# Performance work log

Measured on AMD Instinct MI355X. Metric: run time of the kernel, lower is better.

The kernel has to match this reference:

```python
import jax, jax.numpy as jnp
import numpy as np
import math

# dims: batch, seq_len, d_model, heads, head_dim
B, L, DM, H, DH = 1, 4096, 1024, 16, 64
BS, W, MAXD, DFF = 64, 16, 256, 4096  # block_size, band width (blocks), max rel distance, ffn dim
NB = L // BS


def _static_layout():
    # Static block-sparse causal band layout: tgt block n attends to src blocks [n-W+1 .. n].
    # Mirrors construct_blocksparse_rel_ids: rel = tgt_pos - src_pos, pos ids start at 1
    # (0 reserved for padding), clamp rel<-1 -> -1, rel>max_distance -> max_distance, then +1.
    n = np.arange(NB)[:, None, None, None]
    w = np.arange(W)[None, :, None, None]
    i = np.arange(BS)[None, None, :, None]
    j = np.arange(BS)[None, None, None, :]
    src_blk = n - (W - 1) + w
    # valid: block exists; diagonal block (w==W-1) is causal within-block (j<=i)
    valid = (src_blk >= 0) & ((w < W - 1) | (j <= i))
    tgt_pos = n * BS + i + 1
    src_pos = np.clip(src_blk, 0, None) * BS + j + 1
    rel = np.clip(tgt_pos - src_pos, -1, MAXD) + 1
    rel = np.where(valid, rel, 0)  # masked positions get rel id 0 (as in masked_fill_)
    src_idx = np.clip(np.arange(NB)[:, None] - (W - 1) + np.arange(W)[None, :], 0, None)
    return jnp.asarray(rel), jnp.asarray(valid), jnp.asarray(src_idx)

REL_IDS, VALID, SRC_IDX = _static_layout()  # [NB,W,BS,BS], [NB,W,BS,BS], [NB,W]


def _ln(x, g, b):
    m = x.mean(-1, keepdims=True)
    v = ((x - m) ** 2).mean(-1, keepdims=True)
    return (x - m) * jax.lax.rsqrt(v + 1e-5) * g + b


def setup_inputs() -> dict:
    key = jax.random.key(0)
    ks = jax.random.split(key, 10)
    p = lambda k, shape: jax.random.normal(k, shape, jnp.float32) * 0.02
    return dict(
        x=jax.random.normal(ks[0], (B, L, DM), jnp.float32),
        Wq=p(ks[1], (DM, DM)), Wk=p(ks[2], (DM, DM)), Wv=p(ks[3], (DM, DM)),
        Wo=p(ks[4], (DM, DM)),
        rel_emb=p(ks[5], (MAXD + 2, H)),  # per-head relative position bias table
        ln1_g=jnp.ones((DM,), jnp.float32), ln1_b=jnp.zeros((DM,), jnp.float32),
        ln2_g=jnp.ones((DM,), jnp.float32), ln2_b=jnp.zeros((DM,), jnp.float32),
        W1=p(ks[6], (DM, DFF)), b1=jnp.zeros((DFF,), jnp.float32),
        W2=p(ks[7], (DFF, DM)), b2=jnp.zeros((DM,), jnp.float32),
    )


def reference(x, Wq, Wk, Wv, Wo, rel_emb, ln1_g, ln1_b, ln2_g, ln2_b, W1, b1, W2, b2):
    h = _ln(x, ln1_g, ln1_b)

    def heads(Wt):
        return (h @ Wt).reshape(B, NB, BS, H, DH).transpose(0, 3, 1, 2, 4)  # [B,H,NB,BS,DH]

    q, k, v = heads(Wq), heads(Wk), heads(Wv)
    k_band = k[:, :, SRC_IDX]  # gather nonzero src blocks -> [B,H,NB,W,BS,DH]
    v_band = v[:, :, SRC_IDX]
    scores = jnp.einsum('bhnid,bhnwjd->bhniwj', q, k_band) / math.sqrt(DH)
    # relative position bias, per block pair and head
    bias = rel_emb[REL_IDS].transpose(4, 0, 2, 1, 3)  # [H,NB,BS,W,BS]
    scores = scores + bias[None]
    mask = VALID.transpose(0, 2, 1, 3)  # [NB,BS,W,BS]
    scores = jnp.where(mask, scores, jnp.float32(-1e30))
    p = jax.nn.softmax(scores.reshape(B, H, NB, BS, W * BS), axis=-1)
    p = p.reshape(B, H, NB, BS, W, BS)
    o = jnp.einsum('bhniwj,bhnwjd->bhnid', p, v_band)
    o = o.transpose(0, 2, 3, 1, 4).reshape(B, L, DM) @ Wo
    x = x + o
    h2 = _ln(x, ln2_g, ln2_b)
    x = x + (jax.nn.gelu(h2 @ W1 + b1) @ W2 + b2)
    return x
```

## Files before the change

### kernel.cpp

```cpp
#include <hip/hip_runtime.h>
#include <math.h>

typedef __bf16 bf16x8 __attribute__((ext_vector_type(8)));
typedef float  f32x4  __attribute__((ext_vector_type(4)));
typedef short  s16x8  __attribute__((ext_vector_type(8)));

__device__ __forceinline__ unsigned short f2bf(float f) {
    unsigned int u = __float_as_uint(f);
    u += 0x7fffu + ((u >> 16) & 1u);
    return (unsigned short)(u >> 16);
}

__device__ __forceinline__ float gelu_tanh(float x) {
    float x3 = x * x * x;
    float t = tanhf(0.7978845608028654f * (x + 0.044715f * x3));
    return 0.5f * x * (1.0f + t);
}

__global__ __launch_bounds__(256) void tcvt_kernel(const float* __restrict__ in,
                                                   unsigned short* __restrict__ out,
                                                   int K, int N) {
    __shared__ float tile[32][33];
    int tx = threadIdx.x, ty = threadIdx.y;
    int k0 = blockIdx.y * 32, n0 = blockIdx.x * 32;
#pragma unroll
    for (int s = 0; s < 4; ++s)
        tile[ty + s * 8][tx] = in[(size_t)(k0 + ty + s * 8) * N + n0 + tx];
    __syncthreads();
#pragma unroll
    for (int s = 0; s < 4; ++s)
        out[(size_t)(n0 + ty + s * 8) * K + k0 + tx] = f2bf(tile[tx][ty + s * 8]);
}

__global__ __launch_bounds__(256) void ln_kernel(const float* __restrict__ x,
                                                 const float* __restrict__ g,
                                                 const float* __restrict__ b,
                                                 unsigned short* __restrict__ out) {
    int row = blockIdx.x;
    int tid = threadIdx.x;
    float4 v = ((const float4*)(x + (size_t)row * 1024))[tid];
    float s  = v.x + v.y + v.z + v.w;
    float ss = v.x * v.x + v.y * v.y + v.z * v.z + v.w * v.w;
#pragma unroll
    for (int o = 32; o > 0; o >>= 1) { s += __shfl_down(s, o); ss += __shfl_down(ss, o); }
    __shared__ float red[8];
    if ((tid & 63) == 0) { red[(tid >> 6) * 2] = s; red[(tid >> 6) * 2 + 1] = ss; }
    __syncthreads();
    s  = red[0] + red[2] + red[4] + red[6];
    ss = red[1] + red[3] + red[5] + red[7];
    float mean = s * (1.0f / 1024.0f);
    float var  = ss * (1.0f / 1024.0f) - mean * mean;
    float rs   = rsqrtf(var + 1e-5f);
    float4 gv = ((const float4*)g)[tid];
    float4 bv = ((const float4*)b)[tid];
    ushort4 o4;
    o4.x = f2bf((v.x - mean) * rs * gv.x + bv.x);
    o4.y = f2bf((v.y - mean) * rs * gv.y + bv.y);
    o4.z = f2bf((v.z - mean) * rs * gv.z + bv.z);
    o4.w = f2bf((v.w - mean) * rs * gv.w + bv.w);
    ((ushort4*)(out + (size_t)row * 1024))[tid] = o4;
}

__global__ __launch_bounds__(256) void tvt_kernel(const unsigned short* __restrict__ in,
                                                  unsigned short* __restrict__ out) {
    __shared__ unsigned short tile[64][72];
    int t = threadIdx.x;
    int l0 = blockIdx.x * 64, c0 = blockIdx.y * 64;
    int tr = t >> 3, tc = (t & 7) * 8;
#pragma unroll
    for (int s = 0; s < 2; ++s) {
        int r = tr + s * 32;
        s16x8 v = *(const s16x8*)(in + (size_t)(l0 + r) * 3072 + 2048 + c0 + tc);
        *(s16x8*)(&tile[r][tc]) = v;
    }
    __syncthreads();
#pragma unroll
    for (int s = 0; s < 2; ++s) {
        int c = tr + s * 32;
        s16x8 w;
#pragma unroll
        for (int e = 0; e < 8; ++e) w[e] = (short)tile[tc + e][c];
        *(s16x8*)(out + (size_t)(c0 + c) * 4096 + l0 + tc) = w;
    }
}

#define BM 128
#define BN 128
#define BKK 64

template <int EPI>
__global__ __launch_bounds__(256) void gemm_kernel(const unsigned short* __restrict__ A,
                                                   const unsigned short* __restrict__ Bt,
                                                   void* __restrict__ C,
                                                   const float* __restrict__ bias,
                                                   const float* __restrict__ resid,
                                                   int M, int N, int K) {
    __shared__ __align__(16) unsigned short sA[BM * BKK];
    __shared__ __align__(16) unsigned short sB[BN * BKK];

    const int tid  = threadIdx.x;
    const int wv   = tid >> 6;
    const int lane = tid & 63;
    const int wr   = wv >> 1, wc = wv & 1;
    const int lg   = lane >> 4;
    const int l15  = lane & 15;

    const int brow = blockIdx.y * BM;
    const int bcol = blockIdx.x * BN;

    f32x4 acc[4][4] = {};

    const int l8 = lane >> 3;
    const int lc = (lane & 7) * 8;

    for (int kt = 0; kt < K; kt += BKK) {
        __syncthreads();
#pragma unroll
        for (int q = 0; q < 4; ++q) {
            int ch = 4 * wv + q;
            const unsigned short* srcA = A + (size_t)(brow + 8 * ch + l8) * K + kt + lc;
            __builtin_amdgcn_global_load_lds((const __attribute__((address_space(1))) void*)srcA,
                                             (__attribute__((address_space(3))) void*)(sA + ch * 512),
                                             16, 0, 0);
        }
#pragma unroll
        for (int q = 0; q < 4; ++q) {
            int ch = 4 * wv + q;
            const unsigned short* srcB = Bt + (size_t)(bcol + 8 * ch + l8) * K + kt + lc;
            __builtin_amdgcn_global_load_lds((const __attribute__((address_space(1))) void*)srcB,
                                             (__attribute__((address_space(3))) void*)(sB + ch * 512),
                                             16, 0, 0);
        }
        __syncthreads();

        bf16x8 af[4][2], bfr[4][2];
#pragma unroll
        for (int mi = 0; mi < 4; ++mi)
#pragma unroll
            for (int kk = 0; kk < 2; ++kk)
                af[mi][kk] = *(const bf16x8*)(sA + (wr * 64 + mi * 16 + l15) * BKK + lg * 8 + kk * 32);
#pragma unroll
        for (int ni = 0; ni < 4; ++ni)
#pragma unroll
            for (int kk = 0; kk < 2; ++kk)
                bfr[ni][kk] = *(const bf16x8*)(sB + (wc * 64 + ni * 16 + l15) * BKK + lg * 8 + kk * 32);

#pragma unroll
        for (int kk = 0; kk < 2; ++kk)
#pragma unroll
            for (int mi = 0; mi < 4; ++mi)
#pragma unroll
                for (int ni = 0; ni < 4; ++ni)
                    acc[mi][ni] = __builtin_amdgcn_mfma_f32_16x16x32_bf16(af[mi][kk], bfr[ni][kk],
                                                                          acc[mi][ni], 0, 0, 0);
    }

#pragma unroll
    for (int mi = 0; mi < 4; ++mi)
#pragma unroll
        for (int ni = 0; ni < 4; ++ni)
#pragma unroll
            for (int r = 0; r < 4; ++r) {
                int row = brow + wr * 64 + mi * 16 + lg * 4 + r;
                int col = bcol + wc * 64 + ni * 16 + l15;
                size_t idx = (size_t)row * N + col;
                float v = acc[mi][ni][r];
                if (EPI == 0) {
                    ((unsigned short*)C)[idx] = f2bf(v);
                } else if (EPI == 1) {
                    ((float*)C)[idx] = v + resid[idx];
                } else if (EPI == 2) {
                    v += bias[col];
                    ((unsigned short*)C)[idx] = f2bf(gelu_tanh(v));
                } else {
                    ((float*)C)[idx] = v + bias[col] + resid[idx];
                }
            }
}

__device__ __forceinline__ void stage64(const unsigned short* __restrict__ mat, int ld,
                                        int grow0, int kcol,
                                        unsigned short* lds_tile, int q, int wave, int lane) {
    const int l8 = lane >> 3;
    const int sc = ((lane & 7) ^ l8) << 3;
    const unsigned short* src = mat + (size_t)(grow0 + q * 64 + wave * 8 + l8) * ld + kcol + sc;
    unsigned short* dst = lds_tile + ((q * 64 + wave * 8) << 6);
    __builtin_amdgcn_global_load_lds((const __attribute__((address_space(1))) void*)src,
                                     (__attribute__((address_space(3))) void*)dst, 16, 0, 0);
}

__device__ __forceinline__ bf16x8 ldfrag(const unsigned short* tile, int row, int chunk) {
    return *(const bf16x8*)(tile + (row << 6) + (((chunk ^ row) & 7) << 3));
}

template <int EPI>
__global__ __launch_bounds__(512, 2) void gemm256_kernel(
        const unsigned short* __restrict__ A, int lda,
        const unsigned short* __restrict__ Bt, int ldb,
        void* __restrict__ Cv, const float* __restrict__ bias,
        int ldc, int NT, int gm, int gn, unsigned long long slab_stride) {
    extern __shared__ unsigned short lds[];
    unsigned short* sA = lds;
    unsigned short* sB = lds + 2 * 256 * 64;

    const int tid  = threadIdx.x;
    const int wave = tid >> 6, lane = tid & 63;
    const int wr = wave >> 2, wc = wave & 3;
    const int lg = lane >> 4, l15 = lane & 15;

    const int nwg = gridDim.x;
    const int bid = blockIdx.x;
    const int q8 = nwg >> 3, r8 = nwg & 7;
    const int xcd = bid & 7, loc = bid >> 3;
    const int swz = (xcd < r8 ? xcd * (q8 + 1) : r8 * (q8 + 1) + (xcd - r8) * q8) + loc;
    const int split = swz / (gm * gn);
    const int rem   = swz % (gm * gn);
    const int brow = (rem / gn) << 8;
    const int bcol = (rem % gn) << 8;
    const int kbase = split * (NT << 6);

    f32x4 acc[8][4] = {};

#define STAGE_A(tt, q_, pbuf) stage64(A, lda, brow, kbase + ((tt) << 6), sA + (pbuf) * 16384, (q_), wave, lane)
#define STAGE_B(tt, q_, pbuf) stage64(Bt, ldb, bcol, kbase + ((tt) << 6), sB + (pbuf) * 16384, (q_), wave, lane)

    STAGE_A(0, 0, 0); STAGE_A(0, 1, 0); STAGE_A(0, 2, 0); STAGE_A(0, 3, 0);
    STAGE_B(0, 0, 0); STAGE_B(0, 1, 0); STAGE_B(0, 2, 0); STAGE_B(0, 3, 0);
    STAGE_A(1, 0, 1); STAGE_A(1, 1, 1); STAGE_A(1, 2, 1); STAGE_A(1, 3, 1);
    STAGE_B(1, 0, 1); STAGE_B(1, 1, 1);
    asm volatile("s_waitcnt vmcnt(6)" ::: "memory");
    __builtin_amdgcn_s_barrier();

    for (int t = 0; t < NT; ++t) {
        const int p = t & 1;
        const unsigned short* tA = sA + p * 16384;
        const unsigned short* tB = sB + p * 16384;
        bf16x8 a0[4][2], a1[4][2], b0[2][2], b1[2][2];

#pragma unroll
        for (int im = 0; im < 4; ++im)
#pragma unroll
            for (int kk = 0; kk < 2; ++kk)
                a0[im][kk] = ldfrag(tA, wr * 128 + im * 16 + l15, lg + kk * 4);
#pragma unroll
        for (int in = 0; in < 2; ++in)
#pragma unroll
            for (int kk = 0; kk < 2; ++kk)
                b0[in][kk] = ldfrag(tB, wc * 64 + in * 16 + l15, lg + kk * 4);
        if (t + 1 < NT) { STAGE_B(t + 1, 2, p ^ 1); STAGE_B(t + 1, 3, p ^ 1); }
        __builtin_amdgcn_s_barrier();
        asm volatile("s_waitcnt lgkmcnt(0)" ::: "memory");
        __builtin_amdgcn_sched_barrier(0);
        __builtin_amdgcn_s_setprio(1);
#pragma unroll
        for (int kk = 0; kk < 2; ++kk)
#pragma unroll
            for (int im = 0; im < 4; ++im)
#pragma unroll
                for (int in = 0; in < 2; ++in)
                    acc[im][in] = __builtin_amdgcn_mfma_f32_16x16x32_bf16(a0[im][kk], b0[in][kk], acc[im][in], 0, 0, 0);
        __builtin_amdgcn_s_setprio(0);
        __builtin_amdgcn_s_barrier();

#pragma unroll
        for (int im = 0; im < 4; ++im)
#pragma unroll
            for (int kk = 0; kk < 2; ++kk)
                a1[im][kk] = ldfrag(tA, wr * 128 + 64 + im * 16 + l15, lg + kk * 4);
        if (t + 2 < NT) { STAGE_A(t + 2, 0, p); STAGE_A(t + 2, 2, p); }
        __builtin_amdgcn_s_barrier();
        asm volatile("s_waitcnt lgkmcnt(0)" ::: "memory");
        __builtin_amdgcn_sched_barrier(0);
        __builtin_amdgcn_s_setprio(1);
#pragma unroll
        for (int kk = 0; kk < 2; ++kk)
#pragma unroll
            for (int im = 0; im < 4; ++im)
#pragma unroll
                for (int in = 0; in < 2; ++in)
                    acc[4 + im][in] = __builtin_amdgcn_mfma_f32_16x16x32_bf16(a1[im][kk], b0[in][kk], acc[4 + im][in], 0, 0, 0);
        __builtin_amdgcn_s_setprio(0);
        __builtin_amdgcn_s_barrier();

#pragma unroll
        for (int in = 0; in < 2; ++in)
#pragma unroll
            for (int kk = 0; kk < 2; ++kk)
                b1[in][kk] = ldfrag(tB, wc * 64 + 32 + in * 16 + l15, lg + kk * 4);
        if (t + 2 < NT) { STAGE_A(t + 2, 1, p); STAGE_A(t + 2, 3, p); }
        __builtin_amdgcn_s_barrier();
        asm volatile("s_waitcnt lgkmcnt(0)" ::: "memory");
        __builtin_amdgcn_sched_barrier(0);
        __builtin_amdgcn_s_setprio(1);
#pragma unroll
        for (int kk = 0; kk < 2; ++kk)
#pragma unroll
            for (int im = 0; im < 4; ++im)
#pragma unroll
                for (int in = 0; in < 2; ++in)
                    acc[4 + im][2 + in] = __builtin_amdgcn_mfma_f32_16x16x32_bf16(a1[im][kk], b1[in][kk], acc[4 + im][2 + in], 0, 0, 0);
        __builtin_amdgcn_s_setprio(0);
        __builtin_amdgcn_s_barrier();

        if (t + 2 < NT) { STAGE_B(t + 2, 0, p); STAGE_B(t + 2, 1, p); }
        __builtin_amdgcn_s_barrier();
        asm volatile("s_waitcnt lgkmcnt(0)" ::: "memory");
        __builtin_amdgcn_sched_barrier(0);
        __builtin_amdgcn_s_setprio(1);
#pragma unroll
        for (int kk = 0; kk < 2; ++kk)
#pragma unroll
            for (int im = 0; im < 4; ++im)
#pragma unroll
                for (int in = 0; in < 2; ++in)
                    acc[im][2 + in] = __builtin_amdgcn_mfma_f32_16x16x32_bf16(a0[im][kk], b1[in][kk], acc[im][2 + in], 0, 0, 0);
        __builtin_amdgcn_s_setprio(0);
        if (t + 2 < NT) asm volatile("s_waitcnt vmcnt(6)" ::: "memory");
        else            asm volatile("s_waitcnt vmcnt(0)" ::: "memory");
        __builtin_amdgcn_s_barrier();
    }
#undef STAGE_A
#undef STAGE_B

#pragma unroll
    for (int mi = 0; mi < 8; ++mi)
#pragma unroll
        for (int ni = 0; ni < 4; ++ni)
#pragma unroll
            for (int rr = 0; rr < 4; ++rr) {
                int row = brow + wr * 128 + mi * 16 + lg * 4 + rr;
                int col = bcol + wc * 64 + ni * 16 + l15;
                float v = acc[mi][ni][rr];
                if (EPI == 0) {
                    ((unsigned short*)Cv)[(size_t)row * ldc + col] = f2bf(v);
                } else if (EPI == 2) {
                    v += bias[col];
                    ((unsigned short*)Cv)[(size_t)row * ldc + col] = f2bf(gelu_tanh(v));
                } else {
                    ((unsigned short*)Cv)[slab_stride * split + (size_t)row * ldc + col] = f2bf(v);
                }
            }
}

__global__ __launch_bounds__(256) void reduce4_kernel(const unsigned short* __restrict__ part,
                                                      const float* __restrict__ bias,
                                                      const float* __restrict__ resid,
                                                      float* __restrict__ out) {
    int i4 = blockIdx.x * 256 + threadIdx.x;
    float4 r  = ((const float4*)resid)[i4];
    float4 bb = ((const float4*)bias)[i4 & 255];
    float s0 = r.x + bb.x, s1 = r.y + bb.y, s2 = r.z + bb.z, s3 = r.w + bb.w;
#pragma unroll
    for (int s = 0; s < 4; ++s) {
        ushort4 u = ((const ushort4*)(part + (size_t)s * 4194304))[i4];
        s0 += __uint_as_float((unsigned)u.x << 16);
        s1 += __uint_as_float((unsigned)u.y << 16);
        s2 += __uint_as_float((unsigned)u.z << 16);
        s3 += __uint_as_float((unsigned)u.w << 16);
    }
    float4 o; o.x = s0; o.y = s1; o.z = s2; o.w = s3;
    ((float4*)out)[i4] = o;
}

__device__ __forceinline__ void stage8(const unsigned short* __restrict__ src_row0, int ld,
                                       unsigned short* ldsdst, int lane) {
    const int r8 = lane >> 3;
    const int c  = (lane & 7) ^ r8;
    const unsigned short* src = src_row0 + (size_t)r8 * ld + c * 8;
    __builtin_amdgcn_global_load_lds((const __attribute__((address_space(1))) void*)src,
                                     (__attribute__((address_space(3))) void*)ldsdst, 16, 0, 0);
}

__global__ __launch_bounds__(256, 2) void attn2_kernel(const unsigned short* __restrict__ qkv,
                                                       const unsigned short* __restrict__ vt,
                                                       const float* __restrict__ rel_emb,
                                                       unsigned short* __restrict__ outp) {
    const int lid   = blockIdx.y * gridDim.x + blockIdx.x;
    const int rid   = (lid & 7) * 64 + (lid >> 3);
    const int h     = rid >> 5;
    const int strip = rid & 31;
    const int n0    = strip * 2;

    const int tid  = threadIdx.x;
    const int wv   = tid >> 6;
    const int lane = tid & 63;
    const int qb   = wv >> 1;
    const int half = wv & 1;
    const int lg   = lane >> 4;
    const int l15  = lane & 15;
    const int nq   = n0 + qb;

    __shared__ __align__(16) unsigned short sK[2][4096];
    __shared__ __align__(16) unsigned short sV[2][4096];
    __shared__ __align__(16) unsigned short sP[4][2048];
    __shared__ float sRelF[258];

    unsigned short* sQ  = &sP[0][0];
    unsigned short* sPw = &sP[wv][0];

    for (int i = tid; i < 258; i += 256) sRelF[i] = rel_emb[i * 16 + h];
    const float relC = rel_emb[257 * 16 + h];

    const int tlo = (n0 >= 15) ? 0 : (15 - n0);

#pragma unroll
    for (int s = 0; s < 4; ++s) {
        int r0 = wv * 32 + s * 8;
        stage8(qkv + (size_t)(n0 * 64 + r0) * 3072 + h * 64, 3072, sQ + r0 * 64, lane);
    }
    {
        const int src = n0 - 15 + tlo;
#pragma unroll
        for (int s = 0; s < 2; ++s) {
            int r0 = wv * 16 + s * 8;
            stage8(qkv + (size_t)(src * 64 + r0) * 3072 + 1024 + h * 64, 3072, &sK[0][r0 * 64], lane);
            stage8(vt + (size_t)(h * 64 + r0) * 4096 + src * 64, 4096, &sV[0][r0 * 64], lane);
        }
    }
    asm volatile("s_waitcnt vmcnt(4)" ::: "memory");
    __builtin_amdgcn_s_barrier();

    bf16x8 qf[2][2];
#pragma unroll
    for (int mi = 0; mi < 2; ++mi)
#pragma unroll
        for (int kk = 0; kk < 2; ++kk)
            qf[mi][kk] = ldfrag(sQ, qb * 64 + half * 32 + mi * 16 + l15, lg + kk * 4);
    asm volatile("s_waitcnt lgkmcnt(0)" ::: "memory");
    __builtin_amdgcn_sched_barrier(0);
    __builtin_amdgcn_s_barrier();

    f32x4 oacc[2][4] = {};
    float mrow[2][4], lrow[2][4];
#pragma unroll
    for (int mi = 0; mi < 2; ++mi)
#pragma unroll
        for (int rr = 0; rr < 4; ++rr) { mrow[mi][rr] = -1e30f; lrow[mi][rr] = 0.f; }

    for (int t = tlo; t <= 16; ++t) {
        const int cur = (t - tlo) & 1;
        if (t < 16) {
            const int src = n0 - 15 + (t + 1);
#pragma unroll
            for (int s = 0; s < 2; ++s) {
                int r0 = wv * 16 + s * 8;
                stage8(qkv + (size_t)(src * 64 + r0) * 3072 + 1024 + h * 64, 3072, &sK[cur ^ 1][r0 * 64], lane);
                stage8(vt + (size_t)(h * 64 + r0) * 4096 + src * 64, 4096, &sV[cur ^ 1][r0 * 64], lane);
            }
            asm volatile("s_waitcnt vmcnt(4)" ::: "memory");
        } else {
            asm volatile("s_waitcnt vmcnt(0)" ::: "memory");
        }
        __builtin_amdgcn_s_barrier();

        const bool act = (t >= qb) && (t - qb <= 15);
        if (act) {
            const unsigned short* tK = &sK[cur][0];
            const unsigned short* tV = &sV[cur][0];
            const int woff = 15 + qb - t;

            f32x4 s[2][4] = {};
            __builtin_amdgcn_s_setprio(1);
#pragma unroll
            for (int jt = 0; jt < 4; ++jt) {
                bf16x8 kf0 = ldfrag(tK, jt * 16 + l15, lg);
                bf16x8 kf1 = ldfrag(tK, jt * 16 + l15, lg + 4);
#pragma unroll
                for (int mi = 0; mi < 2; ++mi) {
                    s[mi][jt] = __builtin_amdgcn_mfma_f32_16x16x32_bf16(qf[mi][0], kf0, s[mi][jt], 0, 0, 0);
                    s[mi][jt] = __builtin_amdgcn_mfma_f32_16x16x32_bf16(qf[mi][1], kf1, s[mi][jt], 0, 0, 0);
                }
            }
            __builtin_amdgcn_s_setprio(0);

            float pm[2][4];
#pragma unroll
            for (int mi = 0; mi < 2; ++mi)
#pragma unroll
                for (int rr = 0; rr < 4; ++rr) pm[mi][rr] = -1e30f;

            if (woff >= 5) {
#pragma unroll
                for (int mi = 0; mi < 2; ++mi)
#pragma unroll
                    for (int jt = 0; jt < 4; ++jt)
#pragma unroll
                        for (int rr = 0; rr < 4; ++rr) {
                            float v = s[mi][jt][rr] * 0.125f + relC;
                            s[mi][jt][rr] = v;
                            pm[mi][rr] = fmaxf(pm[mi][rr], v);
                        }
            } else if (woff > 0) {
#pragma unroll
                for (int mi = 0; mi < 2; ++mi)
#pragma unroll
                    for (int jt = 0; jt < 4; ++jt)
#pragma unroll
                        for (int rr = 0; rr < 4; ++rr) {
                            int i = half * 32 + mi * 16 + lg * 4 + rr;
                            int j = jt * 16 + l15;
                            int relid = min(woff * 64 + i - j, 256) + 1;
                            float v = s[mi][jt][rr] * 0.125f + sRelF[relid];
                            s[mi][jt][rr] = v;
                            pm[mi][rr] = fmaxf(pm[mi][rr], v);
                        }
            } else {
#pragma unroll
                for (int mi = 0; mi < 2; ++mi)
#pragma unroll
                    for (int jt = 0; jt < 4; ++jt)
#pragma unroll
                        for (int rr = 0; rr < 4; ++rr) {
                            int i = half * 32 + mi * 16 + lg * 4 + rr;
                            int j = jt * 16 + l15;
                            float v = (j <= i) ? (s[mi][jt][rr] * 0.125f + sRelF[i - j + 1]) : -1e30f;
                            s[mi][jt][rr] = v;
                            pm[mi][rr] = fmaxf(pm[mi][rr], v);
                        }
            }

            float scl[2][4], rs[2][4];
#pragma unroll
            for (int mi = 0; mi < 2; ++mi)
#pragma unroll
                for (int rr = 0; rr < 4; ++rr) {
                    float v = pm[mi][rr];
                    v = fmaxf(v, __shfl_xor(v, 1)); v = fmaxf(v, __shfl_xor(v, 2));
                    v = fmaxf(v, __shfl_xor(v, 4)); v = fmaxf(v, __shfl_xor(v, 8));
                    float mn = fmaxf(mrow[mi][rr], v);
                    scl[mi][rr] = __expf(mrow[mi][rr] - mn);
                    mrow[mi][rr] = mn;
                    rs[mi][rr] = 0.f;
                }
#pragma unroll
            for (int mi = 0; mi < 2; ++mi)
#pragma unroll
                for (int jt = 0; jt < 4; ++jt)
#pragma unroll
                    for (int rr = 0; rr < 4; ++rr) {
                        float p = __expf(s[mi][jt][rr] - mrow[mi][rr]);
                        rs[mi][rr] += p;
                        int row = mi * 16 + lg * 4 + rr, col = jt * 16 + l15;
                        sPw[(row << 6) + ((((col >> 3) ^ row) & 7) << 3) + (col & 7)] = f2bf(p);
                    }
#pragma unroll
            for (int mi = 0; mi < 2; ++mi)
#pragma unroll
                for (int rr = 0; rr < 4; ++rr) {
                    float v = rs[mi][rr];
                    v += __shfl_xor(v, 1); v += __shfl_xor(v, 2);
                    v += __shfl_xor(v, 4); v += __shfl_xor(v, 8);
                    lrow[mi][rr] = lrow[mi][rr] * scl[mi][rr] + v;
                }
#pragma unroll
            for (int mi = 0; mi < 2; ++mi)
#pragma unroll
                for (int dt = 0; dt < 4; ++dt)
#pragma unroll
                    for (int rr = 0; rr < 4; ++rr)
                        oacc[mi][dt][rr] *= scl[mi][rr];

            bf16x8 pf[2][2];
#pragma unroll
            for (int mi = 0; mi < 2; ++mi)
#pragma unroll
                for (int kk = 0; kk < 2; ++kk)
                    pf[mi][kk] = ldfrag(sPw, mi * 16 + l15, lg + kk * 4);
            __builtin_amdgcn_s_setprio(1);
#pragma unroll
            for (int dt = 0; dt < 4; ++dt) {
                bf16x8 vf0 = ldfrag(tV, dt * 16 + l15, lg);
                bf16x8 vf1 = ldfrag(tV, dt * 16 + l15, lg + 4);
#pragma unroll
                for (int mi = 0; mi < 2; ++mi) {
                    oacc[mi][dt] = __builtin_amdgcn_mfma_f32_16x16x32_bf16(pf[mi][0], vf0, oacc[mi][dt], 0, 0, 0);
                    oacc[mi][dt] = __builtin_amdgcn_mfma_f32_16x16x32_bf16(pf[mi][1], vf1, oacc[mi][dt], 0, 0, 0);
                }
            }
            __builtin_amdgcn_s_setprio(0);
        }
        __builtin_amdgcn_s_barrier();
    }

#pragma unroll
    for (int mi = 0; mi < 2; ++mi)
#pragma unroll
        for (int rr = 0; rr < 4; ++rr) {
            float inv = 1.0f / lrow[mi][rr];
#pragma unroll
            for (int dt = 0; dt < 4; ++dt) {
                size_t row = (size_t)(nq * 64 + half * 32 + mi * 16 + lg * 4 + rr);
                outp[row * 1024 + h * 64 + dt * 16 + l15] = f2bf(oacc[mi][dt][rr] * inv);
            }
        }
}

extern "C" void kernel_launch(void* const* d_in, const int* in_sizes, int n_in,
                              void* d_out, int out_size, void* d_ws, size_t ws_size,
                              hipStream_t stream) {
    const float* x    = (const float*)d_in[0];
    const float* Wq   = (const float*)d_in[1];
    const float* Wk   = (const float*)d_in[2];
    const float* Wv   = (const float*)d_in[3];
    const float* Wo   = (const float*)d_in[4];
    const float* rel  = (const float*)d_in[5];
    const float* ln1g = (const float*)d_in[6];
    const float* ln1b = (const float*)d_in[7];
    const float* ln2g = (const float*)d_in[8];
    const float* ln2b = (const float*)d_in[9];
    const float* W1   = (const float*)d_in[10];
    const float* b1   = (const float*)d_in[11];
    const float* W2   = (const float*)d_in[12];
    const float* b2   = (const float*)d_in[13];

    char* ws = (char*)d_ws;
    unsigned short* wqkvT = (unsigned short*)(ws + 0);
    unsigned short* woT   = (unsigned short*)(ws + 6291456);
    unsigned short* attnb = (unsigned short*)(ws + 8388608);
    unsigned short* w1T   = (unsigned short*)(ws + 16777216);
    unsigned short* hbuf  = (unsigned short*)(ws + 25165824);
    unsigned short* w2T   = (unsigned short*)(ws + 33554432);
    float*          x2    = (float*)(ws + 41943040);
    unsigned short* qkv   = (unsigned short*)(ws + 58720256);
    unsigned short* vt    = (unsigned short*)(ws + 83886080);
    unsigned short* gbuf  = (unsigned short*)(ws + 58720256);
    unsigned short* part  = (unsigned short*)(ws + 0);

    const int smem = 131072;
    hipFuncSetAttribute((const void*)gemm256_kernel<0>, hipFuncAttributeMaxDynamicSharedMemorySize, smem);
    hipFuncSetAttribute((const void*)gemm256_kernel<2>, hipFuncAttributeMaxDynamicSharedMemorySize, smem);
    hipFuncSetAttribute((const void*)gemm256_kernel<4>, hipFuncAttributeMaxDynamicSharedMemorySize, smem);

    dim3 tb(32, 8);
    tcvt_kernel<<<dim3(32, 32), tb, 0, stream>>>(Wq, wqkvT, 1024, 1024);
    tcvt_kernel<<<dim3(32, 32), tb, 0, stream>>>(Wk, wqkvT + 1048576, 1024, 1024);
    tcvt_kernel<<<dim3(32, 32), tb, 0, stream>>>(Wv, wqkvT + 2097152, 1024, 1024);
    tcvt_kernel<<<dim3(32, 32), tb, 0, stream>>>(Wo, woT, 1024, 1024);
    tcvt_kernel<<<dim3(128, 32), tb, 0, stream>>>(W1, w1T, 1024, 4096);
    tcvt_kernel<<<dim3(32, 128), tb, 0, stream>>>(W2, w2T, 4096, 1024);

    ln_kernel<<<4096, 256, 0, stream>>>(x, ln1g, ln1b, hbuf);

    gemm256_kernel<0><<<192, 512, smem, stream>>>(hbuf, 1024, wqkvT, 1024, qkv,
                                                  nullptr, 3072, 16, 16, 12, 0ULL);

    tvt_kernel<<<dim3(64, 16), 256, 0, stream>>>(qkv, vt);

    attn2_kernel<<<dim3(32, 16), 256, 0, stream>>>(qkv, vt, rel, attnb);

    gemm_kernel<1><<<dim3(1024 / 128, 4096 / 128), 256, 0, stream>>>(attnb, woT, x2,
                                                                     nullptr, x, 4096, 1024, 1024);

    ln_kernel<<<4096, 256, 0, stream>>>(x2, ln2g, ln2b, hbuf);

    gemm256_kernel<2><<<256, 512, smem, stream>>>(hbuf, 1024, w1T, 1024, gbuf,
                                                  b1, 4096, 16, 16, 16, 0ULL);

    gemm256_kernel<4><<<256, 512, smem, stream>>>(gbuf, 4096, w2T, 4096, part,
                                                  nullptr, 1024, 16, 16, 4, 4194304ULL);

    reduce4_kernel<<<4096, 256, 0, stream>>>(part, b2, x2, (float*)d_out);
}
```

Measured before the change: 263.1 us.

## Restructure attention to register-resident P and route Wo through split-K GEMM

Rewrites the attention kernel to use 512 threads, with each wave owning 16 query rows. Scores are computed transposed (K·Q), so each lane holds one query row. Probabilities are packed to bf16 in registers and fed directly into 16x16x16 MFMAs for P·V, which removes the LDS round-trip for P and the cross-lane shuffles for row max and sum. Output goes through an LDS staging tile for wide stores. The Wo projection switches from the simple 128x128 GEMM to the 256-tile split-K GEMM plus a reduce kernel, trading an extra bf16 partial buffer and a launch for better GEMM efficiency.

```diff
diff --git a/kernel.cpp b/kernel.cpp
--- a/kernel.cpp
+++ b/kernel.cpp
@@ -2,6 +2,7 @@
 #include <math.h>
 
 typedef __bf16 bf16x8 __attribute__((ext_vector_type(8)));
+typedef short  s16x4  __attribute__((ext_vector_type(4)));
 typedef float  f32x4  __attribute__((ext_vector_type(4)));
 typedef short  s16x8  __attribute__((ext_vector_type(8)));
 
@@ -9,6 +10,25 @@
     unsigned int u = __float_as_uint(f);
     u += 0x7fffu + ((u >> 16) & 1u);
     return (unsigned short)(u >> 16);
+}
+
+__device__ __forceinline__ unsigned cvt_pk_bf16(float a, float b) {
+    unsigned r;
+    asm volatile("v_cvt_pk_bf16_f32 %0, %1, %2" : "=v"(r) : "v"(a), "v"(b));
+    return r;
+}
+
+__device__ __forceinline__ f32x4 mfma16(s16x4 a, s16x4 b, f32x4 c) {
+#if __has_builtin(__builtin_amdgcn_mfma_f32_16x16x16bf16_1k)
+    return __builtin_amdgcn_mfma_f32_16x16x16bf16_1k(a, b, c, 0, 0, 0);
+#else
+    asm volatile("s_nop 3\n\t"
+                 "v_mfma_f32_16x16x16_bf16 %0, %1, %2, %0\n\t"
+                 "s_nop 7\n\t"
+                 "s_nop 7"
+                 : "+v"(c) : "v"(a), "v"(b));
+    return c;
+#endif
 }
 
 __device__ __forceinline__ float gelu_tanh(float x) {
@@ -84,98 +104,13 @@
     }
 }
 
-#define BM 128
-#define BN 128
-#define BKK 64
-
-template <int EPI>
-__global__ __launch_bounds__(256) void gemm_kernel(const unsigned short* __restrict__ A,
-                                                   const unsigned short* __restrict__ Bt,
-                                                   void* __restrict__ C,
-                                                   const float* __restrict__ bias,
-                                                   const float* __restrict__ resid,
-                                                   int M, int N, int K) {
-    __shared__ __align__(16) unsigned short sA[BM * BKK];
-    __shared__ __align__(16) unsigned short sB[BN * BKK];
-
-    const int tid  = threadIdx.x;
-    const int wv   = tid >> 6;
-    const int lane = tid & 63;
-    const int wr   = wv >> 1, wc = wv & 1;
-    const int lg   = lane >> 4;
-    const int l15  = lane & 15;
-
-    const int brow = blockIdx.y * BM;
-    const int bcol = blockIdx.x * BN;
-
-    f32x4 acc[4][4] = {};
-
-    const int l8 = lane >> 3;
-    const int lc = (lane & 7) * 8;
-
-    for (int kt = 0; kt < K; kt += BKK) {
-        __syncthreads();
-#pragma unroll
-        for (int q = 0; q < 4; ++q) {
-            int ch = 4 * wv + q;
-            const unsigned short* srcA = A + (size_t)(brow + 8 * ch + l8) * K + kt + lc;
-            __builtin_amdgcn_global_load_lds((const __attribute__((address_space(1))) void*)srcA,
-                                             (__attribute__((address_space(3))) void*)(sA + ch * 512),
-                                             16, 0, 0);
-        }
-#pragma unroll
-        for (int q = 0; q < 4; ++q) {
-            int ch = 4 * wv + q;
-            const unsigned short* srcB = Bt + (size_t)(bcol + 8 * ch + l8) * K + kt + lc;
-            __builtin_amdgcn_global_load_lds((const __attribute__((address_space(1))) void*)srcB,
-                                             (__attribute__((address_space(3))) void*)(sB + ch * 512),
-                                             16, 0, 0);
-        }
-        __syncthreads();
-
-        bf16x8 af[4][2], bfr[4][2];
-#pragma unroll
-        for (int mi = 0; mi < 4; ++mi)
-#pragma unroll
-            for (int kk = 0; kk < 2; ++kk)
-                af[mi][kk] = *(const bf16x8*)(sA + (wr * 64 + mi * 16 + l15) * BKK + lg * 8 + kk * 32);
-#pragma unroll
-        for (int ni = 0; ni < 4; ++ni)
-#pragma unroll
-            for (int kk = 0; kk < 2; ++kk)
-                bfr[ni][kk] = *(const bf16x8*)(sB + (wc * 64 + ni * 16 + l15) * BKK + lg * 8 + kk * 32);
-
-#pragma unroll
-        for (int kk = 0; kk < 2; ++kk)
-#pragma unroll
-            for (int mi = 0; mi < 4; ++mi)
-#pragma unroll
-                for (int ni = 0; ni < 4; ++ni)
-                    acc[mi][ni] = __builtin_amdgcn_mfma_f32_16x16x32_bf16(af[mi][kk], bfr[ni][kk],
-                                                                          acc[mi][ni], 0, 0, 0);
-    }
-
-#pragma unroll
-    for (int mi = 0; mi < 4; ++mi)
-#pragma unroll
-        for (int ni = 0; ni < 4; ++ni)
-#pragma unroll
-            for (int r = 0; r < 4; ++r) {
-                int row = brow + wr * 64 + mi * 16 + lg * 4 + r;
-                int col = bcol + wc * 64 + ni * 16 + l15;
-                size_t idx = (size_t)row * N + col;
-                float v = acc[mi][ni][r];
-                if (EPI == 0) {
-                    ((unsigned short*)C)[idx] = f2bf(v);
-                } else if (EPI == 1) {
-                    ((float*)C)[idx] = v + resid[idx];
-                } else if (EPI == 2) {
-                    v += bias[col];
-                    ((unsigned short*)C)[idx] = f2bf(gelu_tanh(v));
-                } else {
-                    ((float*)C)[idx] = v + bias[col] + resid[idx];
-                }
-            }
+__device__ __forceinline__ void stage8(const unsigned short* __restrict__ src_row0, int ld,
+                                       unsigned short* ldsdst, int lane) {
+    const int r8 = lane >> 3;
+    const int c  = (lane & 7) ^ r8;
+    const unsigned short* src = src_row0 + (size_t)r8 * ld + c * 8;
+    __builtin_amdgcn_global_load_lds((const __attribute__((address_space(1))) void*)src,
+                                     (__attribute__((address_space(3))) void*)ldsdst, 16, 0, 0);
 }
 
 __device__ __forceinline__ void stage64(const unsigned short* __restrict__ mat, int ld,
@@ -191,6 +126,10 @@
 
 __device__ __forceinline__ bf16x8 ldfrag(const unsigned short* tile, int row, int chunk) {
     return *(const bf16x8*)(tile + (row << 6) + (((chunk ^ row) & 7) << 3));
+}
+
+__device__ __forceinline__ s16x4 ldfrag64(const unsigned short* tile, int row, int ch16, int half) {
+    return *(const s16x4*)(tile + (row << 6) + (((ch16 ^ row) & 7) << 3) + (half << 2));
 }
 
 template <int EPI>
@@ -342,14 +281,18 @@
             }
 }
 
+template <int HB>
 __global__ __launch_bounds__(256) void reduce4_kernel(const unsigned short* __restrict__ part,
                                                       const float* __restrict__ bias,
                                                       const float* __restrict__ resid,
                                                       float* __restrict__ out) {
     int i4 = blockIdx.x * 256 + threadIdx.x;
     float4 r  = ((const float4*)resid)[i4];
-    float4 bb = ((const float4*)bias)[i4 & 255];
-    float s0 = r.x + bb.x, s1 = r.y + bb.y, s2 = r.z + bb.z, s3 = r.w + bb.w;
+    float s0 = r.x, s1 = r.y, s2 = r.z, s3 = r.w;
+    if (HB) {
+        float4 bb = ((const float4*)bias)[i4 & 255];
+        s0 += bb.x; s1 += bb.y; s2 += bb.z; s3 += bb.w;
+    }
 #pragma unroll
     for (int s = 0; s < 4; ++s) {
         ushort4 u = ((const ushort4*)(part + (size_t)s * 4194304))[i4];
@@ -362,16 +305,7 @@
     ((float4*)out)[i4] = o;
 }
 
-__device__ __forceinline__ void stage8(const unsigned short* __restrict__ src_row0, int ld,
-                                       unsigned short* ldsdst, int lane) {
-    const int r8 = lane >> 3;
-    const int c  = (lane & 7) ^ r8;
-    const unsigned short* src = src_row0 + (size_t)r8 * ld + c * 8;
-    __builtin_amdgcn_global_load_lds((const __attribute__((address_space(1))) void*)src,
-                                     (__attribute__((address_space(3))) void*)ldsdst, 16, 0, 0);
-}
-
-__global__ __launch_bounds__(256, 2) void attn2_kernel(const unsigned short* __restrict__ qkv,
+__global__ __launch_bounds__(512, 4) void attn3_kernel(const unsigned short* __restrict__ qkv,
                                                        const unsigned short* __restrict__ vt,
                                                        const float* __restrict__ rel_emb,
                                                        unsigned short* __restrict__ outp) {
@@ -384,70 +318,45 @@
     const int tid  = threadIdx.x;
     const int wv   = tid >> 6;
     const int lane = tid & 63;
-    const int qb   = wv >> 1;
-    const int half = wv & 1;
+    const int qb   = wv >> 2;
     const int lg   = lane >> 4;
     const int l15  = lane & 15;
-    const int nq   = n0 + qb;
+    const int iq   = (wv & 3) * 16 + l15;
+    const int q0   = n0 * 64 + wv * 16;
 
     __shared__ __align__(16) unsigned short sK[2][4096];
     __shared__ __align__(16) unsigned short sV[2][4096];
-    __shared__ __align__(16) unsigned short sP[4][2048];
     __shared__ float sRelF[258];
 
-    unsigned short* sQ  = &sP[0][0];
-    unsigned short* sPw = &sP[wv][0];
-
-    for (int i = tid; i < 258; i += 256) sRelF[i] = rel_emb[i * 16 + h];
+    bf16x8 qf[2];
+    {
+        const unsigned short* qrow = qkv + (size_t)(q0 + l15) * 3072 + h * 64 + lg * 8;
+        qf[0] = *(const bf16x8*)(qrow);
+        qf[1] = *(const bf16x8*)(qrow + 32);
+    }
+
+    for (int i = tid; i < 258; i += 512) sRelF[i] = rel_emb[i * 16 + h];
     const float relC = rel_emb[257 * 16 + h];
 
     const int tlo = (n0 >= 15) ? 0 : (15 - n0);
-
-#pragma unroll
-    for (int s = 0; s < 4; ++s) {
-        int r0 = wv * 32 + s * 8;
-        stage8(qkv + (size_t)(n0 * 64 + r0) * 3072 + h * 64, 3072, sQ + r0 * 64, lane);
-    }
     {
         const int src = n0 - 15 + tlo;
-#pragma unroll
-        for (int s = 0; s < 2; ++s) {
-            int r0 = wv * 16 + s * 8;
-            stage8(qkv + (size_t)(src * 64 + r0) * 3072 + 1024 + h * 64, 3072, &sK[0][r0 * 64], lane);
-            stage8(vt + (size_t)(h * 64 + r0) * 4096 + src * 64, 4096, &sV[0][r0 * 64], lane);
-        }
-    }
-    asm volatile("s_waitcnt vmcnt(4)" ::: "memory");
+        stage8(qkv + (size_t)(src * 64 + wv * 8) * 3072 + 1024 + h * 64, 3072, &sK[0][wv * 8 * 64], lane);
+        stage8(vt + (size_t)(h * 64 + wv * 8) * 4096 + src * 64, 4096, &sV[0][wv * 8 * 64], lane);
+    }
+    asm volatile("s_waitcnt lgkmcnt(0)" ::: "memory");
     __builtin_amdgcn_s_barrier();
 
-    bf16x8 qf[2][2];
-#pragma unroll
-    for (int mi = 0; mi < 2; ++mi)
-#pragma unroll
-        for (int kk = 0; kk < 2; ++kk)
-            qf[mi][kk] = ldfrag(sQ, qb * 64 + half * 32 + mi * 16 + l15, lg + kk * 4);
-    asm volatile("s_waitcnt lgkmcnt(0)" ::: "memory");
-    __builtin_amdgcn_sched_barrier(0);
-    __builtin_amdgcn_s_barrier();
-
-    f32x4 oacc[2][4] = {};
-    float mrow[2][4], lrow[2][4];
-#pragma unroll
-    for (int mi = 0; mi < 2; ++mi)
-#pragma unroll
-        for (int rr = 0; rr < 4; ++rr) { mrow[mi][rr] = -1e30f; lrow[mi][rr] = 0.f; }
+    f32x4 oacc[4] = {};
+    float mrow = -3e38f, lrow = 0.f;
 
     for (int t = tlo; t <= 16; ++t) {
         const int cur = (t - tlo) & 1;
         if (t < 16) {
             const int src = n0 - 15 + (t + 1);
-#pragma unroll
-            for (int s = 0; s < 2; ++s) {
-                int r0 = wv * 16 + s * 8;
-                stage8(qkv + (size_t)(src * 64 + r0) * 3072 + 1024 + h * 64, 3072, &sK[cur ^ 1][r0 * 64], lane);
-                stage8(vt + (size_t)(h * 64 + r0) * 4096 + src * 64, 4096, &sV[cur ^ 1][r0 * 64], lane);
-            }
-            asm volatile("s_waitcnt vmcnt(4)" ::: "memory");
+            stage8(qkv + (size_t)(src * 64 + wv * 8) * 3072 + 1024 + h * 64, 3072, &sK[cur ^ 1][wv * 8 * 64], lane);
+            stage8(vt + (size_t)(h * 64 + wv * 8) * 4096 + src * 64, 4096, &sV[cur ^ 1][wv * 8 * 64], lane);
+            asm volatile("s_waitcnt vmcnt(2)" ::: "memory");
         } else {
             asm volatile("s_waitcnt vmcnt(0)" ::: "memory");
         }
@@ -459,122 +368,85 @@
             const unsigned short* tV = &sV[cur][0];
             const int woff = 15 + qb - t;
 
-            f32x4 s[2][4] = {};
+            f32x4 st[4] = {};
             __builtin_amdgcn_s_setprio(1);
 #pragma unroll
             for (int jt = 0; jt < 4; ++jt) {
                 bf16x8 kf0 = ldfrag(tK, jt * 16 + l15, lg);
                 bf16x8 kf1 = ldfrag(tK, jt * 16 + l15, lg + 4);
-#pragma unroll
-                for (int mi = 0; mi < 2; ++mi) {
-                    s[mi][jt] = __builtin_amdgcn_mfma_f32_16x16x32_bf16(qf[mi][0], kf0, s[mi][jt], 0, 0, 0);
-                    s[mi][jt] = __builtin_amdgcn_mfma_f32_16x16x32_bf16(qf[mi][1], kf1, s[mi][jt], 0, 0, 0);
-                }
+                st[jt] = __builtin_amdgcn_mfma_f32_16x16x32_bf16(kf0, qf[0], st[jt], 0, 0, 0);
+                st[jt] = __builtin_amdgcn_mfma_f32_16x16x32_bf16(kf1, qf[1], st[jt], 0, 0, 0);
             }
             __builtin_amdgcn_s_setprio(0);
 
-            float pm[2][4];
-#pragma unroll
-            for (int mi = 0; mi < 2; ++mi)
-#pragma unroll
-                for (int rr = 0; rr < 4; ++rr) pm[mi][rr] = -1e30f;
-
+            float pm = -3e38f;
             if (woff >= 5) {
 #pragma unroll
-                for (int mi = 0; mi < 2; ++mi)
-#pragma unroll
-                    for (int jt = 0; jt < 4; ++jt)
-#pragma unroll
-                        for (int rr = 0; rr < 4; ++rr) {
-                            float v = s[mi][jt][rr] * 0.125f + relC;
-                            s[mi][jt][rr] = v;
-                            pm[mi][rr] = fmaxf(pm[mi][rr], v);
-                        }
+                for (int jt = 0; jt < 4; ++jt)
+#pragma unroll
+                    for (int rr = 0; rr < 4; ++rr) {
+                        float v = st[jt][rr] * 0.125f + relC;
+                        st[jt][rr] = v;
+                        pm = fmaxf(pm, v);
+                    }
             } else if (woff > 0) {
 #pragma unroll
-                for (int mi = 0; mi < 2; ++mi)
-#pragma unroll
-                    for (int jt = 0; jt < 4; ++jt)
-#pragma unroll
-                        for (int rr = 0; rr < 4; ++rr) {
-                            int i = half * 32 + mi * 16 + lg * 4 + rr;
-                            int j = jt * 16 + l15;
-                            int relid = min(woff * 64 + i - j, 256) + 1;
-                            float v = s[mi][jt][rr] * 0.125f + sRelF[relid];
-                            s[mi][jt][rr] = v;
-                            pm[mi][rr] = fmaxf(pm[mi][rr], v);
-                        }
+                for (int jt = 0; jt < 4; ++jt)
+#pragma unroll
+                    for (int rr = 0; rr < 4; ++rr) {
+                        int j = jt * 16 + lg * 4 + rr;
+                        int relid = min(woff * 64 + iq - j, 256) + 1;
+                        float v = st[jt][rr] * 0.125f + sRelF[relid];
+                        st[jt][rr] = v;
+                        pm = fmaxf(pm, v);
+                    }
             } else {
 #pragma unroll
-                for (int mi = 0; mi < 2; ++mi)
-#pragma unroll
-                    for (int jt = 0; jt < 4; ++jt)
-#pragma unroll
-                        for (int rr = 0; rr < 4; ++rr) {
-                            int i = half * 32 + mi * 16 + lg * 4 + rr;
-                            int j = jt * 16 + l15;
-                            float v = (j <= i) ? (s[mi][jt][rr] * 0.125f + sRelF[i - j + 1]) : -1e30f;
-                            s[mi][jt][rr] = v;
-                            pm[mi][rr] = fmaxf(pm[mi][rr], v);
-                        }
+                for (int jt = 0; jt < 4; ++jt)
+#pragma unroll
+                    for (int rr = 0; rr < 4; ++rr) {
+                        int j = jt * 16 + lg * 4 + rr;
+                        float v = (j <= iq) ? (st[jt][rr] * 0.125f + sRelF[iq - j + 1]) : -1e30f;
+                        st[jt][rr] = v;
+                        pm = fmaxf(pm, v);
+                    }
             }
-
-            float scl[2][4], rs[2][4];
-#pragma unroll
-            for (int mi = 0; mi < 2; ++mi)
-#pragma unroll
-                for (int rr = 0; rr < 4; ++rr) {
-                    float v = pm[mi][rr];
-                    v = fmaxf(v, __shfl_xor(v, 1)); v = fmaxf(v, __shfl_xor(v, 2));
-                    v = fmaxf(v, __shfl_xor(v, 4)); v = fmaxf(v, __shfl_xor(v, 8));
-                    float mn = fmaxf(mrow[mi][rr], v);
-                    scl[mi][rr] = __expf(mrow[mi][rr] - mn);
-                    mrow[mi][rr] = mn;
-                    rs[mi][rr] = 0.f;
-                }
-#pragma unroll
-            for (int mi = 0; mi < 2; ++mi)
-#pragma unroll
-                for (int jt = 0; jt < 4; ++jt)
-#pragma unroll
-                    for (int rr = 0; rr < 4; ++rr) {
-                        float p = __expf(s[mi][jt][rr] - mrow[mi][rr]);
-                        rs[mi][rr] += p;
-                        int row = mi * 16 + lg * 4 + rr, col = jt * 16 + l15;
-                        sPw[(row << 6) + ((((col >> 3) ^ row) & 7) << 3) + (col & 7)] = f2bf(p);
-                    }
-#pragma unroll
-            for (int mi = 0; mi < 2; ++mi)
-#pragma unroll
-                for (int rr = 0; rr < 4; ++rr) {
-                    float v = rs[mi][rr];
-                    v += __shfl_xor(v, 1); v += __shfl_xor(v, 2);
-                    v += __shfl_xor(v, 4); v += __shfl_xor(v, 8);
-                    lrow[mi][rr] = lrow[mi][rr] * scl[mi][rr] + v;
-                }
-#pragma unroll
-            for (int mi = 0; mi < 2; ++mi)
-#pragma unroll
-                for (int dt = 0; dt < 4; ++dt)
-#pragma unroll
-                    for (int rr = 0; rr < 4; ++rr)
-                        oacc[mi][dt][rr] *= scl[mi][rr];
-
-            bf16x8 pf[2][2];
-#pragma unroll
-            for (int mi = 0; mi < 2; ++mi)
-#pragma unroll
-                for (int kk = 0; kk < 2; ++kk)
-                    pf[mi][kk] = ldfrag(sPw, mi * 16 + l15, lg + kk * 4);
+            pm = fmaxf(pm, __shfl_xor(pm, 16));
+            pm = fmaxf(pm, __shfl_xor(pm, 32));
+            float mn  = fmaxf(mrow, pm);
+            float scl = __expf(mrow - mn);
+            mrow = mn;
+
+            float rs = 0.f;
+            unsigned pk0[4], pk1[4];
+#pragma unroll
+            for (int jt = 0; jt < 4; ++jt) {
+                float p0 = __expf(st[jt][0] - mn);
+                float p1 = __expf(st[jt][1] - mn);
+                float p2 = __expf(st[jt][2] - mn);
+                float p3 = __expf(st[jt][3] - mn);
+                rs += (p0 + p1) + (p2 + p3);
+                pk0[jt] = cvt_pk_bf16(p0, p1);
+                pk1[jt] = cvt_pk_bf16(p2, p3);
+            }
+            rs += __shfl_xor(rs, 16);
+            rs += __shfl_xor(rs, 32);
+            lrow = lrow * scl + rs;
+#pragma unroll
+            for (int dt = 0; dt < 4; ++dt)
+#pragma unroll
+                for (int rr = 0; rr < 4; ++rr)
+                    oacc[dt][rr] *= scl;
+
             __builtin_amdgcn_s_setprio(1);
 #pragma unroll
-            for (int dt = 0; dt < 4; ++dt) {
-                bf16x8 vf0 = ldfrag(tV, dt * 16 + l15, lg);
-                bf16x8 vf1 = ldfrag(tV, dt * 16 + l15, lg + 4);
-#pragma unroll
-                for (int mi = 0; mi < 2; ++mi) {
-                    oacc[mi][dt] = __builtin_amdgcn_mfma_f32_16x16x32_bf16(pf[mi][0], vf0, oacc[mi][dt], 0, 0, 0);
-                    oacc[mi][dt] = __builtin_amdgcn_mfma_f32_16x16x32_bf16(pf[mi][1], vf1, oacc[mi][dt], 0, 0, 0);
+            for (int ks = 0; ks < 4; ++ks) {
+                union { unsigned u[2]; s16x4 v; } pu;
+                pu.u[0] = pk0[ks]; pu.u[1] = pk1[ks];
+#pragma unroll
+                for (int dt = 0; dt < 4; ++dt) {
+                    s16x4 vf = ldfrag64(tV, dt * 16 + l15, 2 * ks + (lg >> 1), lg & 1);
+                    oacc[dt] = mfma16(vf, pu.v, oacc[dt]);
                 }
             }
             __builtin_amdgcn_s_setprio(0);
@@ -582,17 +454,23 @@
         __builtin_amdgcn_s_barrier();
     }
 
-#pragma unroll
-    for (int mi = 0; mi < 2; ++mi)
-#pragma unroll
-        for (int rr = 0; rr < 4; ++rr) {
-            float inv = 1.0f / lrow[mi][rr];
-#pragma unroll
-            for (int dt = 0; dt < 4; ++dt) {
-                size_t row = (size_t)(nq * 64 + half * 32 + mi * 16 + lg * 4 + rr);
-                outp[row * 1024 + h * 64 + dt * 16 + l15] = f2bf(oacc[mi][dt][rr] * inv);
-            }
+    float inv = 1.0f / lrow;
+    unsigned short* sO = &sK[0][0] + wv * 1024;
+#pragma unroll
+    for (int dt = 0; dt < 4; ++dt)
+#pragma unroll
+        for (int c = 0; c < 2; ++c) {
+            unsigned pr = cvt_pk_bf16(oacc[dt][2 * c] * inv, oacc[dt][2 * c + 1] * inv);
+            int d  = dt * 16 + lg * 4 + 2 * c;
+            int off = (l15 << 6) + ((((d >> 3) ^ (l15 & 7)) & 7) << 3) + (d & 7);
+            *(unsigned*)(sO + off) = pr;
         }
+#pragma unroll
+    for (int c2 = 0; c2 < 2; ++c2) {
+        int ch = lg + 4 * c2;
+        bf16x8 ov = ldfrag(sO, l15, ch);
+        *(s16x8*)(outp + (size_t)(q0 + l15) * 1024 + h * 64 + ch * 8) = *(const s16x8*)&ov;
+    }
 }
 
 extern "C" void kernel_launch(void* const* d_in, const int* in_sizes, int n_in,
@@ -614,17 +492,18 @@
     const float* b2   = (const float*)d_in[13];
 
     char* ws = (char*)d_ws;
-    unsigned short* wqkvT = (unsigned short*)(ws + 0);
-    unsigned short* woT   = (unsigned short*)(ws + 6291456);
-    unsigned short* attnb = (unsigned short*)(ws + 8388608);
-    unsigned short* w1T   = (unsigned short*)(ws + 16777216);
-    unsigned short* hbuf  = (unsigned short*)(ws + 25165824);
-    unsigned short* w2T   = (unsigned short*)(ws + 33554432);
-    float*          x2    = (float*)(ws + 41943040);
-    unsigned short* qkv   = (unsigned short*)(ws + 58720256);
-    unsigned short* vt    = (unsigned short*)(ws + 83886080);
-    unsigned short* gbuf  = (unsigned short*)(ws + 58720256);
-    unsigned short* part  = (unsigned short*)(ws + 0);
+    unsigned short* wqkvT  = (unsigned short*)(ws + 0);
+    unsigned short* woT    = (unsigned short*)(ws + 6291456);
+    unsigned short* attnb  = (unsigned short*)(ws + 8388608);
+    unsigned short* w1T    = (unsigned short*)(ws + 16777216);
+    unsigned short* hbuf   = (unsigned short*)(ws + 25165824);
+    unsigned short* w2T    = (unsigned short*)(ws + 33554432);
+    float*          x2     = (float*)(ws + 41943040);
+    unsigned short* qkv    = (unsigned short*)(ws + 58720256);
+    unsigned short* vt     = (unsigned short*)(ws + 83886080);
+    unsigned short* wopart = (unsigned short*)(ws + 58720256);
+    unsigned short* gbuf   = (unsigned short*)(ws + 58720256);
+    unsigned short* part   = (unsigned short*)(ws + 0);
 
     const int smem = 131072;
     hipFuncSetAttribute((const void*)gemm256_kernel<0>, hipFuncAttributeMaxDynamicSharedMemorySize, smem);
@@ -646,10 +525,11 @@
 
     tvt_kernel<<<dim3(64, 16), 256, 0, stream>>>(qkv, vt);
 
-    attn2_kernel<<<dim3(32, 16), 256, 0, stream>>>(qkv, vt, rel, attnb);
-
-    gemm_kernel<1><<<dim3(1024 / 128, 4096 / 128), 256, 0, stream>>>(attnb, woT, x2,
-                                                                     nullptr, x, 4096, 1024, 1024);
+    attn3_kernel<<<dim3(32, 16), 512, 0, stream>>>(qkv, vt, rel, attnb);
+
+    gemm256_kernel<4><<<256, 512, smem, stream>>>(attnb, 1024, woT, 1024, wopart,
+                                                  nullptr, 1024, 4, 16, 4, 4194304ULL);
+    reduce4_kernel<0><<<4096, 256, 0, stream>>>(wopart, nullptr, x, x2);
 
     ln_kernel<<<4096, 256, 0, stream>>>(x2, ln2g, ln2b, hbuf);
 
@@ -659,5 +539,5 @@
     gemm256_kernel<4><<<256, 512, smem, stream>>>(gbuf, 4096, w2T, 4096, part,
                                                   nullptr, 1024, 16, 16, 4, 4194304ULL);
 
-    reduce4_kernel<<<4096, 256, 0, stream>>>(part, b2, x2, (float*)d_out);
-}
+    reduce4_kernel<1><<<4096, 256, 0, stream>>>(part, b2, x2, (float*)d_out);
+}
```

Result: faster. 246.6 us (-6.3%).
